# Kernel tuning notes

Measured on AMD Instinct MI355X. Metric: run time of the kernel, lower is better.

The kernel has to match this reference:

```python
import jax, jax.numpy as jnp
import numpy as np

PAD = 1
STRIDE = 1


def setup_inputs() -> dict:
    key = jax.random.key(0)
    kx, kw, kb = jax.random.split(key, 3)
    C_IN, C_OUT, K, H, W = 128, 256, 3, 256, 256
    lim = 1.0 / np.sqrt(C_IN * K * K)
    x = jax.random.normal(kx, (C_IN, H, W), dtype=jnp.float32)
    weight = jax.random.uniform(kw, (C_OUT, C_IN, K, K), minval=-lim, maxval=lim, dtype=jnp.float32)
    bias = jax.random.uniform(kb, (C_OUT, 1, 1), minval=-lim, maxval=lim, dtype=jnp.float32)
    return {"x": x, "weight": weight, "bias": bias}


def reference(x, weight, bias):
    # Original does per-channel jnp.pad then a scan-based im2col + einsum
    # 'oijk,ihwjk->ohw'. That is exactly a standard cross-correlation conv,
    # expressed here with the efficient fused primitive (same math).
    out = jax.lax.conv_general_dilated(
        x[None],                      # (1, c, h, w)
        weight,                       # (o, i, k, k)
        window_strides=(STRIDE, STRIDE),
        padding=[(PAD, PAD), (PAD, PAD)],
        dimension_numbers=("NCHW", "OIHW", "NCHW"),
    )[0]                              # (o, h', w')
    return out + bias
```

## Files before the change

### kernel.cpp

```cpp
#include <hip/hip_runtime.h>
#include <hip/hip_bf16.h>
#include <stdint.h>


#define CIN   128
#define COUT  256
#define HH    256
#define WW    256
#define HP    258
#define WP    258
#define XP_ELEMS (HP * WP * CIN)

typedef __attribute__((ext_vector_type(8))) __bf16 bf16x8;
typedef __attribute__((ext_vector_type(4))) float  floatx4;
typedef __attribute__((ext_vector_type(8))) short  short8;

#define AS1 __attribute__((address_space(1)))
#define AS3 __attribute__((address_space(3)))

__global__ __launch_bounds__(256) void prep(const float* __restrict__ x,
                                            const float* __restrict__ w,
                                            unsigned short* __restrict__ xp,
                                            unsigned short* __restrict__ wpk) {
    __shared__ __align__(16) unsigned short tile[64][136];
    const int bid = blockIdx.x;
    const int t   = threadIdx.x;
    if (bid < 1024) {
        int h  = bid >> 2;
        int w0 = (bid & 3) << 6;
        int wl = t & 63, icq = t >> 6;
        const float* src = x + h * WW + w0 + wl;
#pragma unroll
        for (int icb = 0; icb < 32; ++icb) {
            int ic = icb * 4 + icq;
            __hip_bfloat16 b = __float2bfloat16(src[ic * (HH * WW)]);
            tile[wl][ic] = __builtin_bit_cast(unsigned short, b);
        }
        __syncthreads();
        int wl2 = t >> 2, q = t & 3;
        const short8* s8 = (const short8*)&tile[wl2][q * 32];
        short8* d8 = (short8*)(xp + ((size_t)(h + 1) * WP + (w0 + 1) + wl2) * CIN + q * 32);
#pragma unroll
        for (int i = 0; i < 4; ++i) d8[i] = s8[i];
    } else if (bid < 2176) {
        int idx = (bid - 1024) * 256 + t;
        int kk  = idx >> 15;
        int rem = idx & 32767;
        __hip_bfloat16 b = __float2bfloat16(w[rem * 9 + kk]);
        wpk[idx] = __builtin_bit_cast(unsigned short, b);
    } else {
        int cid = (bid - 2176) * 256 + t;
        if (cid < 16448) {
            int p = cid >> 4, oct = cid & 15;
            int hp, wp;
            if (p < 258)      { hp = 0;   wp = p; }
            else if (p < 516) { hp = 257; wp = p - 258; }
            else { int s = p - 516; hp = 1 + (s >> 1); wp = (s & 1) * 257; }
            short8 z = {0, 0, 0, 0, 0, 0, 0, 0};
            *(short8*)(xp + ((size_t)hp * WP + wp) * CIN + oct * 8) = z;
        }
    }
}

__global__ __launch_bounds__(256, 2) void conv_mfma(
    const unsigned short* __restrict__ xp,
    const unsigned short* __restrict__ wpk,
    const float* __restrict__ bias,
    float* __restrict__ out) {
    __shared__ __align__(16) unsigned short x_lds[2 * 16384];

    const int tid  = threadIdx.x;
    const int lane = tid & 63;
    const int wv   = tid >> 6;
    const int l15  = lane & 15;
    const int lg   = lane >> 4;
    const int wave_m = (wv >> 1) << 6;
    const int wave_n = (wv & 1) << 6;

    const int orig = blockIdx.x;
    const int swz  = ((orig & 7) << 7) | (orig >> 3);
    const int m0 = (swz >> 9) << 7;
    const int h  = (swz >> 1) & 255;
    const int w0 = (swz & 1) << 7;

    const int soff = (tid >> 3) * CIN + ((((tid & 7) ^ ((tid >> 3) & 7))) << 3);

#define GLD_A(nb_, src_, i_) \
    __builtin_amdgcn_global_load_lds((const AS1 void*)((src_) + (i_) * 32 * CIN), \
        (AS3 void*)((nb_) + (i_) * 2048 + tid * 8), 16, 0, 0)
#define GLD_B(nb_, src_, i_) \
    __builtin_amdgcn_global_load_lds((const AS1 void*)((src_) + (i_) * 32 * CIN), \
        (AS3 void*)((nb_) + 8192 + (i_) * 2048 + tid * 8), 16, 0, 0)

#define LDX(base_, rb_, ks_) \
    (*(const bf16x8*)((base_) + (((rb_) + l15) << 6) + ((((ks_) * 4 + lg) ^ (l15 & 7)) << 3)))

    auto stage = [&](int buf, int kk, int kh, int kw, int hf) {
        unsigned short* nb = x_lds + buf * 16384;
        const unsigned short* asrc =
            wpk + (size_t)kk * (COUT * CIN) + (size_t)m0 * CIN + hf * 64 + soff;
        const unsigned short* bsrc =
            xp + ((size_t)(h + kh) * WP + (w0 + kw)) * CIN + hf * 64 + soff;
#pragma unroll
        for (int i = 0; i < 4; ++i) GLD_A(nb, asrc, i);
#pragma unroll
        for (int i = 0; i < 4; ++i) GLD_B(nb, bsrc, i);
    };

    floatx4 acc[4][4];
#pragma unroll
    for (int fi = 0; fi < 4; ++fi)
#pragma unroll
        for (int fj = 0; fj < 4; ++fj) {
            floatx4 z = {0.f, 0.f, 0.f, 0.f};
            acc[fi][fj] = z;
        }

    stage(0, 0, 0, 0, 0);
    __syncthreads();

#pragma unroll
    for (int t2 = 0; t2 < 18; ++t2) {
        const int cur = t2 & 1;
        const unsigned short* Ab = x_lds + cur * 16384;
        const unsigned short* Bb = Ab + 8192;

        if (t2 < 17) {
            const int tn  = t2 + 1;
            const int kkn = tn >> 1, hfn = tn & 1;
            const int khn = kkn / 3, kwn = kkn - khn * 3;
            stage(cur ^ 1, kkn, khn, kwn, hfn);
        }

#pragma unroll
        for (int ks = 0; ks < 2; ++ks) {
            bf16x8 a[4], b[4];
#pragma unroll
            for (int fj = 0; fj < 4; ++fj) b[fj] = LDX(Bb, wave_n + fj * 16, ks);
#pragma unroll
            for (int fi = 0; fi < 4; ++fi) a[fi] = LDX(Ab, wave_m + fi * 16, ks);
            __builtin_amdgcn_s_setprio(1);
#pragma unroll
            for (int fi = 0; fi < 4; ++fi)
#pragma unroll
                for (int fj = 0; fj < 4; ++fj)
                    acc[fi][fj] = __builtin_amdgcn_mfma_f32_16x16x32_bf16(
                        a[fi], b[fj], acc[fi][fj], 0, 0, 0);
            __builtin_amdgcn_s_setprio(0);
        }

        __syncthreads();
    }
#undef GLD_A
#undef GLD_B
#undef LDX

    const int nbase = h * WW + w0 + wave_n + l15;
#pragma unroll
    for (int fi = 0; fi < 4; ++fi) {
        int mrow = m0 + wave_m + fi * 16 + lg * 4;
#pragma unroll
        for (int r = 0; r < 4; ++r) {
            float bv = bias[mrow + r];
#pragma unroll
            for (int fj = 0; fj < 4; ++fj)
                out[(size_t)(mrow + r) * (HH * WW) + nbase + fj * 16] = acc[fi][fj][r] + bv;
        }
    }
}

extern "C" void kernel_launch(void* const* d_in, const int* in_sizes, int n_in,
                              void* d_out, int out_size, void* d_ws, size_t ws_size,
                              hipStream_t stream) {
    (void)in_sizes; (void)n_in; (void)out_size; (void)ws_size;
    const float* x    = (const float*)d_in[0];
    const float* w    = (const float*)d_in[1];
    const float* bias = (const float*)d_in[2];
    float* out = (float*)d_out;

    unsigned short* xp  = (unsigned short*)d_ws;
    unsigned short* wpk = xp + XP_ELEMS;

    prep<<<dim3(2241), dim3(256), 0, stream>>>(x, w, xp, wpk);
    conv_mfma<<<dim3(1024), dim3(256), 0, stream>>>(xp, wpk, bias, out);
}
```

Before: 133.1 us.

## Pre-pack weights in MFMA fragment order and load A directly from global

The weight prep now writes bf16 weights already arranged in per-lane MFMA fragment order, so the conv kernel loads A fragments straight from global/L2 into registers instead of staging them through LDS. The block grows to 512 threads covering a full 256-wide output row (128x256 tile), halving the grid and giving more reuse of each staged input tile. LDS now holds only the input tile, and the per-iteration barrier moves to the loop top. The trade-offs are per-wave global loads of weights on the critical path and higher register/occupancy pressure from the 512-thread, 4-wave-per-SIMD launch bounds.

```diff
diff --git a/kernel.cpp b/kernel.cpp
--- a/kernel.cpp
+++ b/kernel.cpp
@@ -21,7 +21,7 @@
 __global__ __launch_bounds__(256) void prep(const float* __restrict__ x,
                                             const float* __restrict__ w,
                                             unsigned short* __restrict__ xp,
-                                            unsigned short* __restrict__ wpk) {
+                                            unsigned short* __restrict__ apk) {
     __shared__ __align__(16) unsigned short tile[64][136];
     const int bid = blockIdx.x;
     const int t   = threadIdx.x;
@@ -44,10 +44,16 @@
         for (int i = 0; i < 4; ++i) d8[i] = s8[i];
     } else if (bid < 2176) {
         int idx = (bid - 1024) * 256 + t;
-        int kk  = idx >> 15;
-        int rem = idx & 32767;
-        __hip_bfloat16 b = __float2bfloat16(w[rem * 9 + kk]);
-        wpk[idx] = __builtin_bit_cast(unsigned short, b);
+        int j  = idx & 7;
+        int l  = (idx >> 3) & 63;
+        int mb = (idx >> 9) & 15;
+        int ks = (idx >> 13) & 1;
+        int hf = (idx >> 14) & 1;
+        int kk = idx >> 15;
+        int o  = mb * 16 + (l & 15);
+        int ch = hf * 64 + ks * 32 + (l >> 4) * 8 + j;
+        __hip_bfloat16 b = __float2bfloat16(w[(o * CIN + ch) * 9 + kk]);
+        apk[idx] = __builtin_bit_cast(unsigned short, b);
     } else {
         int cid = (bid - 2176) * 256 + t;
         if (cid < 16448) {
@@ -62,47 +68,42 @@
     }
 }
 
-__global__ __launch_bounds__(256, 2) void conv_mfma(
+__global__ __launch_bounds__(512, 4) void conv_mfma(
     const unsigned short* __restrict__ xp,
-    const unsigned short* __restrict__ wpk,
+    const unsigned short* __restrict__ apk,
     const float* __restrict__ bias,
     float* __restrict__ out) {
-    __shared__ __align__(16) unsigned short x_lds[2 * 16384];
+    __shared__ __align__(16) unsigned short b_lds[2 * 16384];
 
     const int tid  = threadIdx.x;
     const int lane = tid & 63;
     const int wv   = tid >> 6;
     const int l15  = lane & 15;
     const int lg   = lane >> 4;
-    const int wave_m = (wv >> 1) << 6;
-    const int wave_n = (wv & 1) << 6;
+    const int wave_m = (wv >> 2) << 6;
+    const int wave_n = (wv & 3) << 6;
 
     const int orig = blockIdx.x;
-    const int swz  = ((orig & 7) << 7) | (orig >> 3);
-    const int m0 = (swz >> 9) << 7;
-    const int h  = (swz >> 1) & 255;
-    const int w0 = (swz & 1) << 7;
+    const int swz  = ((orig & 7) << 6) | (orig >> 3);
+    const int m0 = (swz >> 8) << 7;
+    const int h  = swz & 255;
 
     const int soff = (tid >> 3) * CIN + ((((tid & 7) ^ ((tid >> 3) & 7))) << 3);
-
-#define GLD_A(nb_, src_, i_) \
-    __builtin_amdgcn_global_load_lds((const AS1 void*)((src_) + (i_) * 32 * CIN), \
-        (AS3 void*)((nb_) + (i_) * 2048 + tid * 8), 16, 0, 0)
+    const int mb0 = (m0 + wave_m) >> 4;
+
 #define GLD_B(nb_, src_, i_) \
-    __builtin_amdgcn_global_load_lds((const AS1 void*)((src_) + (i_) * 32 * CIN), \
-        (AS3 void*)((nb_) + 8192 + (i_) * 2048 + tid * 8), 16, 0, 0)
-
-#define LDX(base_, rb_, ks_) \
-    (*(const bf16x8*)((base_) + (((rb_) + l15) << 6) + ((((ks_) * 4 + lg) ^ (l15 & 7)) << 3)))
-
-    auto stage = [&](int buf, int kk, int kh, int kw, int hf) {
-        unsigned short* nb = x_lds + buf * 16384;
-        const unsigned short* asrc =
-            wpk + (size_t)kk * (COUT * CIN) + (size_t)m0 * CIN + hf * 64 + soff;
+    __builtin_amdgcn_global_load_lds((const AS1 void*)((src_) + (i_) * 8192), \
+        (AS3 void*)((nb_) + (i_) * 4096 + tid * 8), 16, 0, 0)
+
+#define LDB(Bb_, fj_, ks_) \
+    (*(const bf16x8*)((Bb_) + (((wave_n + (fj_) * 16) + l15) << 6) + \
+                      ((((ks_) * 4 + lg) ^ (l15 & 7)) << 3)))
+#define LDA(f_) (*(const bf16x8*)(apk + (size_t)(f_) * 512 + lane * 8))
+
+    auto stage = [&](int buf, int kh, int kw, int hf) {
+        unsigned short* nb = b_lds + buf * 16384;
         const unsigned short* bsrc =
-            xp + ((size_t)(h + kh) * WP + (w0 + kw)) * CIN + hf * 64 + soff;
-#pragma unroll
-        for (int i = 0; i < 4; ++i) GLD_A(nb, asrc, i);
+            xp + ((size_t)(h + kh) * WP + kw) * CIN + hf * 64 + soff;
 #pragma unroll
         for (int i = 0; i < 4; ++i) GLD_B(nb, bsrc, i);
     };
@@ -116,46 +117,60 @@
             acc[fi][fj] = z;
         }
 
-    stage(0, 0, 0, 0, 0);
+    stage(0, 0, 0, 0);
     __syncthreads();
 
 #pragma unroll
     for (int t2 = 0; t2 < 18; ++t2) {
         const int cur = t2 & 1;
-        const unsigned short* Ab = x_lds + cur * 16384;
-        const unsigned short* Bb = Ab + 8192;
+        const unsigned short* Bb = b_lds + cur * 16384;
+        const int kk = t2 >> 1, hf = t2 & 1;
+        const int fb = ((kk * 2 + hf) * 2) * 16 + mb0;
+
+        if (t2 > 0) __builtin_amdgcn_s_barrier();
+
+        bf16x8 a0[4];
+#pragma unroll
+        for (int fi = 0; fi < 4; ++fi) a0[fi] = LDA(fb + fi);
 
         if (t2 < 17) {
             const int tn  = t2 + 1;
             const int kkn = tn >> 1, hfn = tn & 1;
             const int khn = kkn / 3, kwn = kkn - khn * 3;
-            stage(cur ^ 1, kkn, khn, kwn, hfn);
-        }
-
-#pragma unroll
-        for (int ks = 0; ks < 2; ++ks) {
-            bf16x8 a[4], b[4];
-#pragma unroll
-            for (int fj = 0; fj < 4; ++fj) b[fj] = LDX(Bb, wave_n + fj * 16, ks);
-#pragma unroll
-            for (int fi = 0; fi < 4; ++fi) a[fi] = LDX(Ab, wave_m + fi * 16, ks);
-            __builtin_amdgcn_s_setprio(1);
-#pragma unroll
-            for (int fi = 0; fi < 4; ++fi)
-#pragma unroll
-                for (int fj = 0; fj < 4; ++fj)
-                    acc[fi][fj] = __builtin_amdgcn_mfma_f32_16x16x32_bf16(
-                        a[fi], b[fj], acc[fi][fj], 0, 0, 0);
-            __builtin_amdgcn_s_setprio(0);
-        }
-
-        __syncthreads();
+            stage(cur ^ 1, khn, kwn, hfn);
+        }
+
+        bf16x8 b0[4];
+#pragma unroll
+        for (int fj = 0; fj < 4; ++fj) b0[fj] = LDB(Bb, fj, 0);
+        __builtin_amdgcn_s_setprio(1);
+#pragma unroll
+        for (int fi = 0; fi < 4; ++fi)
+#pragma unroll
+            for (int fj = 0; fj < 4; ++fj)
+                acc[fi][fj] = __builtin_amdgcn_mfma_f32_16x16x32_bf16(
+                    a0[fi], b0[fj], acc[fi][fj], 0, 0, 0);
+        __builtin_amdgcn_s_setprio(0);
+
+        bf16x8 a1[4], b1[4];
+#pragma unroll
+        for (int fi = 0; fi < 4; ++fi) a1[fi] = LDA(fb + 16 + fi);
+#pragma unroll
+        for (int fj = 0; fj < 4; ++fj) b1[fj] = LDB(Bb, fj, 1);
+        __builtin_amdgcn_s_setprio(1);
+#pragma unroll
+        for (int fi = 0; fi < 4; ++fi)
+#pragma unroll
+            for (int fj = 0; fj < 4; ++fj)
+                acc[fi][fj] = __builtin_amdgcn_mfma_f32_16x16x32_bf16(
+                    a1[fi], b1[fj], acc[fi][fj], 0, 0, 0);
+        __builtin_amdgcn_s_setprio(0);
     }
-#undef GLD_A
 #undef GLD_B
-#undef LDX
-
-    const int nbase = h * WW + w0 + wave_n + l15;
+#undef LDB
+#undef LDA
+
+    const int nbase = h * WW + wave_n + l15;
 #pragma unroll
     for (int fi = 0; fi < 4; ++fi) {
         int mrow = m0 + wave_m + fi * 16 + lg * 4;
@@ -179,8 +194,8 @@
     float* out = (float*)d_out;
 
     unsigned short* xp  = (unsigned short*)d_ws;
-    unsigned short* wpk = xp + XP_ELEMS;
-
-    prep<<<dim3(2241), dim3(256), 0, stream>>>(x, w, xp, wpk);
-    conv_mfma<<<dim3(1024), dim3(256), 0, stream>>>(xp, wpk, bias, out);
+    unsigned short* apk = xp + XP_ELEMS;
+
+    prep<<<dim3(2241), dim3(256), 0, stream>>>(x, w, xp, apk);
+    conv_mfma<<<dim3(512), dim3(512), 0, stream>>>(xp, apk, bias, out);
 }
```

New measurement: 141.2 us. 1.06x slower.
